# Performance work log

Measured on AMD Instinct MI355X. Metric: run time of the kernel, lower is better.

## Reference

```python
import jax, jax.numpy as jnp
import numpy as np

# Config mirroring RegionExtractor(__init__ defaults, stage='rcnn')
MIN_SIZE = 25.0
IOU_THRESH = 0.3
SCORE_THRESH = 0.001  # applied as box_score_thresh inside the wrapped FRCNN
MAX_DET = 100         # max_detections_per_image
IMG_SIZE = 800.0
B, N = 8, 2048


def setup_inputs() -> dict:
    key = jax.random.key(0)
    k_c, k_wh, k_s = jax.random.split(key, 3)
    # synthesize realistic xyxy boxes inside an 800x800 image
    centers = jax.random.uniform(k_c, (B, N, 2), minval=0.0, maxval=IMG_SIZE)
    wh = jax.random.uniform(k_wh, (B, N, 2), minval=1.0, maxval=250.0)
    x1y1 = jnp.clip(centers - wh / 2, 0.0, IMG_SIZE)
    x2y2 = jnp.clip(centers + wh / 2, 0.0, IMG_SIZE)
    boxes = jnp.concatenate([x1y1, x2y2], axis=-1).astype(jnp.float32)  # [B,N,4]
    scores = jax.random.uniform(k_s, (B, N), dtype=jnp.float32)          # [B,N]
    return {"boxes": boxes, "scores": scores}


def _box_iou(a, b):
    # a: [N,4], b: [N,4] xyxy -> [N,N] IoU (torchvision convention, no +1)
    area_a = (a[:, 2] - a[:, 0]) * (a[:, 3] - a[:, 1])
    area_b = (b[:, 2] - b[:, 0]) * (b[:, 3] - b[:, 1])
    lt = jnp.maximum(a[:, None, :2], b[None, :, :2])
    rb = jnp.minimum(a[:, None, 2:], b[None, :, 2:])
    wh = jnp.clip(rb - lt, 0.0)
    inter = wh[..., 0] * wh[..., 1]
    return inter / (area_a[:, None] + area_b[None, :] - inter)


def _process_image(boxes, scores):
    # boxes [N,4], scores [N] -> (out [K,4], mask [K])
    n = boxes.shape[0]
    w = boxes[:, 2] - boxes[:, 0]
    h = boxes[:, 3] - boxes[:, 1]
    # remove_small_boxes + score threshold (box_score_thresh in wrapped FRCNN)
    valid = (w >= MIN_SIZE) & (h >= MIN_SIZE) & (scores >= SCORE_THRESH)
    order = jnp.argsort(-jnp.where(valid, scores, -jnp.inf))  # desc, invalid last
    b = boxes[order]
    v = valid[order]
    sup = _box_iou(b, b) > IOU_THRESH  # [N,N]
    idx = jnp.arange(n)

    def body(i, keep):
        suppressed = jnp.any(keep & sup[:, i] & (idx < i))
        return keep.at[i].set(v[i] & ~suppressed)

    keep = jax.lax.fori_loop(0, n, body, jnp.zeros(n, dtype=bool))
    # keep is in score order already; take first MAX_DET kept boxes
    rank = jnp.cumsum(keep) - 1
    sel = keep & (rank < MAX_DET)
    tgt = jnp.where(sel, rank, MAX_DET)  # dump non-selected into scratch row
    out = jnp.zeros((MAX_DET + 1, 4), boxes.dtype).at[tgt].set(b)[:MAX_DET]
    num_kept = jnp.minimum(jnp.sum(keep), MAX_DET)
    mask = jnp.arange(MAX_DET) < num_kept
    return out, mask


def reference(boxes, scores):
    # Per-image filter + NMS + top-k, batched via vmap (padded fixed-shape output:
    # original returns a ragged [sum_k,5]; here rows with mask==False are padding).
    out, mask = jax.vmap(_process_image)(boxes, scores)  # [B,K,4], [B,K]
    b = boxes.shape[0]
    img_idx = jnp.repeat(jnp.arange(b, dtype=boxes.dtype), MAX_DET)[:, None]  # [B*K,1]
    regions = jnp.concatenate([img_idx, out.reshape(b * MAX_DET, 4)], axis=1)  # [B*K,5]
    return regions, mask.reshape(-1)
```

## Files before the change

### kernel.cpp

```cpp
#include <hip/hip_runtime.h>

#define NBOX   2048
#define HALF   1024
#define MAXDET 100
#define NIMG   8
#define POOL   256
#define IOU_MID 0x1.333335p-2

typedef unsigned long long u64;

__device__ __forceinline__ u64 shx64(u64 v, int m) {
    int lo = __shfl_xor((int)(unsigned int)v, m, 64);
    int hi = __shfl_xor((int)(unsigned int)(v >> 32), m, 64);
    return ((u64)(unsigned int)hi << 32) | (unsigned int)lo;
}
__device__ __forceinline__ u64 cmpsel(u64 mine, u64 part, bool take_max) {
    return ((mine > part) == take_max) ? mine : part;
}
__device__ __forceinline__ u64 readlane64(u64 v, int l) {
    unsigned int lo = (unsigned int)__builtin_amdgcn_readlane((int)(unsigned int)v, l);
    unsigned int hi = (unsigned int)__builtin_amdgcn_readlane((int)(v >> 32), l);
    return ((u64)hi << 32) | lo;
}
__device__ __forceinline__ u64 mkkey(float4 v, float s, int i) {
    bool valid = ((v.z - v.x) >= 25.0f) && ((v.w - v.y) >= 25.0f) && (s >= 0.001f);
    unsigned int sk = valid ? __float_as_uint(s) : 0u;
    return ((u64)sk << 32) | (unsigned int)(~i);
}

__global__ __launch_bounds__(1024) void k_all(
    const float* __restrict__ boxes, const float* __restrict__ scores,
    float* __restrict__ out)
{
    __shared__ u64    bufA[NBOX];
    __shared__ u64    bufB[NBOX];
    __shared__ u64    supRow[POOL * 4];
    __shared__ float4 sbox[POOL];
    __shared__ u64    mA[POOL], mB[POOL];
    __shared__ u64    validW[4];
    __shared__ u64    pminS;
    __shared__ int    kposL[MAXDET];
    __shared__ float4 leadersB[MAXDET];
    __shared__ float  leadersA[MAXDET];

    const int g    = threadIdx.x;
    const int lane = g & 63;
    const int wv   = g >> 6;
    const int tl   = g & 511;
    const int hbase = (g >> 9) * HALF;
    const int img  = blockIdx.x;
    const float4* bb4 = (const float4*)boxes + img * NBOX;
    const float*  ss  = scores + img * NBOX;

    const int e0 = 2 * tl;
    u64 k0, k1;
    { float4 v = bb4[hbase + e0];     k0 = mkkey(v, ss[hbase + e0],     hbase + e0);     }
    { float4 v = bb4[hbase + e0 + 1]; k1 = mkkey(v, ss[hbase + e0 + 1], hbase + e0 + 1); }

#define SWAP1(a, b, D) { if ((D) ? ((a) < (b)) : ((a) > (b))) { u64 t_ = (a); (a) = (b); (b) = t_; } }
    { bool D = ((tl & 1) == 0); SWAP1(k0, k1, D) }
    for (int KB = 2; KB <= 64; KB <<= 1) {
        bool D = ((tl & KB) == 0);
        for (int m = KB >> 1; m >= 1; m >>= 1) {
            bool tm = (D == ((lane & m) == 0));
            k0 = cmpsel(k0, shx64(k0, m), tm);
            k1 = cmpsel(k1, shx64(k1, m), tm);
        }
        SWAP1(k0, k1, D)
    }
    int sp = 0;
    for (int K = 256; K <= 1024; K <<= 1) {
        bool D = ((e0 & K) == 0);
        for (int j = K >> 1; j >= 128; j >>= 1) {
            u64* buf = (sp & 1) ? bufB : bufA;
            ++sp;
            buf[hbase + e0] = k0; buf[hbase + e0 + 1] = k1;
            __syncthreads();
            int pe = e0 ^ j;
            u64 p0 = buf[hbase + pe], p1 = buf[hbase + pe + 1];
            bool tm = (D == ((e0 & j) == 0));
            k0 = cmpsel(k0, p0, tm); k1 = cmpsel(k1, p1, tm);
        }
        for (int m = 32; m >= 1; m >>= 1) {
            bool tm = (D == ((lane & m) == 0));
            k0 = cmpsel(k0, shx64(k0, m), tm);
            k1 = cmpsel(k1, shx64(k1, m), tm);
        }
        SWAP1(k0, k1, D)
    }
    bufA[hbase + e0] = k0; bufA[hbase + e0 + 1] = k1;
    __syncthreads();

    const u64* hk = bufA;

    u64 c = 0;
    if (g < POOL) {
        u64 a  = hk[g];
        u64 bq = hk[HALF + (POOL - 1 - g)];
        c = (a > bq) ? a : bq;
        mA[g] = c;
    }
    __syncthreads();
    if (g < POOL) { c = cmpsel(c, mA[g ^ 128], (g & 128) == 0); mB[g] = c; }
    __syncthreads();
    if (g < POOL) {
        c = cmpsel(c, mB[g ^ 64], (g & 64) == 0);
        for (int m = 32; m >= 1; m >>= 1)
            c = cmpsel(c, shx64(c, m), (lane & m) == 0);
        unsigned int idx = ~(unsigned int)c;
        float4 v = bb4[idx];
        sbox[g] = v;
        u64 bal = __ballot(((unsigned int)(c >> 32)) != 0u);
        if (lane == 0) validW[wv] = bal;
        if (g == POOL - 1) pminS = c;
    }
    __syncthreads();

    float4 cb[4];
    float  ca[4];
#pragma unroll
    for (int w = 0; w < 4; ++w) {
        float4 v = sbox[(w << 6) + lane];
        cb[w] = v;
        ca[w] = (v.z - v.x) * (v.w - v.y);
    }

    for (int r = 0; r < POOL / 16; ++r) {
        int i = (r << 4) + wv;
        float4 Li = sbox[i];
        float La = (Li.z - Li.x) * (Li.w - Li.y);
        int w0 = i >> 6;
#pragma unroll
        for (int w = 0; w < 4; ++w) {
            if (w >= w0) {
                int j0 = (w << 6) + lane;
                float iw = fminf(Li.z, cb[w].z) - fmaxf(Li.x, cb[w].x);
                float ih = fminf(Li.w, cb[w].w) - fmaxf(Li.y, cb[w].y);
                iw = fmaxf(iw, 0.0f);
                ih = fmaxf(ih, 0.0f);
                float inter = iw * ih;
                float denom = (La + ca[w]) - inter;
                bool hit = (j0 > i) && ((double)inter > IOU_MID * (double)denom);
                u64 bits = __ballot(hit);
                if (lane == 0) supRow[(i << 2) + w] = bits;
            }
        }
    }
    __syncthreads();

    if (g >= 64) return;

    float* regions = out;
    float* maskv   = out + (size_t)NIMG * MAXDET * 5;

    u64 rd0 = supRow[(((0 << 6) + lane) << 2) + 0];
    u64 rd1 = supRow[(((1 << 6) + lane) << 2) + 1];
    u64 rd2 = supRow[(((2 << 6) + lane) << 2) + 2];
    u64 rd3 = supRow[(((3 << 6) + lane) << 2) + 3];

    int nkept = 0;
    u64 pend = 0;
#pragma unroll
    for (int s = 0; s < 4; ++s) {
        u64 rds = (s == 0) ? rd0 : (s == 1) ? rd1 : (s == 2) ? rd2 : rd3;
        u64 mcur = validW[s] & ~readlane64(pend, s);
        int n0 = nkept;
        while (mcur != 0ULL) {
            int il = (int)__builtin_ctzll(mcur);
            if (lane == 0) kposL[nkept] = (s << 6) + il;
            nkept++;
            if (nkept >= MAXDET) break;
            u64 rowS = readlane64(rds, il);
            mcur = (mcur & (mcur - 1)) & ~rowS;
        }
        if (nkept >= MAXDET) break;
        if (s < 3) {
            for (int t = n0 + (lane >> 2); t < nkept; t += 16)
                pend |= supRow[(kposL[t] << 2) + (lane & 3)];
            pend |= shx64(pend, 4);
            pend |= shx64(pend, 8);
            pend |= shx64(pend, 16);
            pend |= shx64(pend, 32);
        }
    }

    for (int t = lane; t < nkept; t += 64) {
        int ip = kposL[t];
        float4 v = sbox[ip];
        float* rr = regions + ((size_t)(img * MAXDET + t)) * 5;
        rr[0] = (float)img; rr[1] = v.x; rr[2] = v.y; rr[3] = v.z; rr[4] = v.w;
        maskv[img * MAXDET + t] = 1.0f;
        leadersB[t] = v;
        leadersA[t] = (v.z - v.x) * (v.w - v.y);
    }

    if (nkept < MAXDET) {
        u64 pmin = pminS;
        int q0 = 0, q1 = 0;
#pragma unroll
        for (int w = 0; w < 16; ++w) {
            q0 += __popcll(__ballot(hk[(w << 6) + lane] >= pmin));
            q1 += __popcll(__ballot(hk[HALF + (w << 6) + lane] >= pmin));
        }
        for (;;) {
            const int lenA = HALF - q0, lenB = HALF - q1;
            const int rem  = lenA + lenB;
            if (rem <= 0) break;
            u64  myKey = 0;
            bool fromA = false;
            if (lane < rem) {
                int lo = lane + 1 - lenB; if (lo < 0) lo = 0;
                int hi = (lane + 1 < lenA) ? lane + 1 : lenA;
                while (lo < hi) {
                    int a = (lo + hi) >> 1, b = lane + 1 - a;
                    if (a < lenA && b > 0 && hk[q0 + a] > hk[HALF + q1 + b - 1]) lo = a + 1;
                    else hi = a;
                }
                int a = lo, b = lane + 1 - a;
                u64 ka = (a > 0) ? hk[q0 + a - 1] : ~0ULL;
                u64 kb = (b > 0) ? hk[HALF + q1 + b - 1] : ~0ULL;
                fromA = (ka < kb);
                myKey = fromA ? ka : kb;
            }
            bool validC = (lane < rem) && (((unsigned int)(myKey >> 32)) != 0u);
            u64 vmask = __ballot(validC);
            float4 v = make_float4(0.0f, 0.0f, 0.0f, 0.0f);
            float varea = 0.0f;
            if (validC) {
                v = bb4[~(unsigned int)myKey];
                varea = (v.z - v.x) * (v.w - v.y);
            }
            bool supL = false;
#pragma unroll 4
            for (int t = 0; t < nkept; ++t) {
                float4 Lb = leadersB[t];
                float  La = leadersA[t];
                float iw = fminf(Lb.z, v.z) - fmaxf(Lb.x, v.x);
                float ih = fminf(Lb.w, v.w) - fmaxf(Lb.y, v.y);
                iw = fmaxf(iw, 0.0f);
                ih = fmaxf(ih, 0.0f);
                float inter = iw * ih;
                float denom = (La + varea) - inter;
                supL = supL || ((double)inter > IOU_MID * (double)denom);
            }
            u64 mcur = vmask & ~__ballot(supL);
            while (mcur != 0ULL) {
                int il = (int)__builtin_ctzll(mcur);
                float bx = __shfl(v.x, il, 64), by = __shfl(v.y, il, 64);
                float bz = __shfl(v.z, il, 64), bw = __shfl(v.w, il, 64);
                float ba = __shfl(varea, il, 64);
                if (lane == il) {
                    float* rr = regions + ((size_t)(img * MAXDET + nkept)) * 5;
                    rr[0] = (float)img; rr[1] = v.x; rr[2] = v.y; rr[3] = v.z; rr[4] = v.w;
                    maskv[img * MAXDET + nkept] = 1.0f;
                    leadersB[nkept] = v;
                    leadersA[nkept] = varea;
                }
                nkept++;
                if (nkept >= MAXDET) break;
                float iw = fminf(bz, v.z) - fmaxf(bx, v.x);
                float ih = fminf(bw, v.w) - fmaxf(by, v.y);
                iw = fmaxf(iw, 0.0f);
                ih = fmaxf(ih, 0.0f);
                float inter = iw * ih;
                float denom = (ba + varea) - inter;
                bool hit = ((double)inter > IOU_MID * (double)denom);
                mcur = (mcur & (mcur - 1)) & ~__ballot(hit);
            }
            if (nkept >= MAXDET) break;
            int nv = __popcll(vmask);
            if (nv < 64) break;
            int nA = __popcll(vmask & __ballot(fromA));
            q0 += nA;
            q1 += nv - nA;
        }
    }

    for (int r = nkept + lane; r < MAXDET; r += 64) {
        float* rr = regions + ((size_t)(img * MAXDET + r)) * 5;
        rr[0] = (float)img; rr[1] = 0.0f; rr[2] = 0.0f; rr[3] = 0.0f; rr[4] = 0.0f;
        maskv[img * MAXDET + r] = 0.0f;
    }
}

extern "C" void kernel_launch(void* const* d_in, const int* in_sizes, int n_in,
                              void* d_out, int out_size, void* d_ws, size_t ws_size,
                              hipStream_t stream) {
    const float* boxes  = (const float*)d_in[0];
    const float* scores = (const float*)d_in[1];
    float* out = (float*)d_out;
    k_all<<<NIMG, 1024, 0, stream>>>(boxes, scores, out);
}
```

Before: 76.38 us.

## Sort four keys per thread with fewer barriers and stage boxes in LDS

The per-half bitonic sort now uses 512 threads holding four keys each. More compare steps happen in registers and wave shuffles, so fewer LDS exchange rounds and __syncthreads are needed. The other 512 threads copy all 2048 boxes of the image into shared memory at the same time, and the later gathers by sorted index read from LDS instead of global memory. This adds 32KB of LDS, which may limit occupancy, though there is only one block per image anyway. It also leaves half the block idle during the sort phase.

```diff
diff --git a/kernel.cpp b/kernel.cpp
--- a/kernel.cpp
+++ b/kernel.cpp
@@ -34,6 +34,7 @@
 {
     __shared__ u64    bufA[NBOX];
     __shared__ u64    bufB[NBOX];
+    __shared__ float4 boxLds[NBOX];
     __shared__ u64    supRow[POOL * 4];
     __shared__ float4 sbox[POOL];
     __shared__ u64    mA[POOL], mB[POOL];
@@ -46,49 +47,87 @@
     const int g    = threadIdx.x;
     const int lane = g & 63;
     const int wv   = g >> 6;
-    const int tl   = g & 511;
-    const int hbase = (g >> 9) * HALF;
     const int img  = blockIdx.x;
     const float4* bb4 = (const float4*)boxes + img * NBOX;
     const float*  ss  = scores + img * NBOX;
 
-    const int e0 = 2 * tl;
-    u64 k0, k1;
-    { float4 v = bb4[hbase + e0];     k0 = mkkey(v, ss[hbase + e0],     hbase + e0);     }
-    { float4 v = bb4[hbase + e0 + 1]; k1 = mkkey(v, ss[hbase + e0 + 1], hbase + e0 + 1); }
-
 #define SWAP1(a, b, D) { if ((D) ? ((a) < (b)) : ((a) > (b))) { u64 t_ = (a); (a) = (b); (b) = t_; } }
-    { bool D = ((tl & 1) == 0); SWAP1(k0, k1, D) }
-    for (int KB = 2; KB <= 64; KB <<= 1) {
-        bool D = ((tl & KB) == 0);
-        for (int m = KB >> 1; m >= 1; m >>= 1) {
-            bool tm = (D == ((lane & m) == 0));
-            k0 = cmpsel(k0, shx64(k0, m), tm);
-            k1 = cmpsel(k1, shx64(k1, m), tm);
-        }
-        SWAP1(k0, k1, D)
-    }
-    int sp = 0;
-    for (int K = 256; K <= 1024; K <<= 1) {
-        bool D = ((e0 & K) == 0);
-        for (int j = K >> 1; j >= 128; j >>= 1) {
-            u64* buf = (sp & 1) ? bufB : bufA;
-            ++sp;
-            buf[hbase + e0] = k0; buf[hbase + e0 + 1] = k1;
-            __syncthreads();
-            int pe = e0 ^ j;
-            u64 p0 = buf[hbase + pe], p1 = buf[hbase + pe + 1];
-            bool tm = (D == ((e0 & j) == 0));
-            k0 = cmpsel(k0, p0, tm); k1 = cmpsel(k1, p1, tm);
-        }
+
+    u64 k0 = 0, k1 = 0, k2 = 0, k3 = 0;
+    int u = 0, hb = 0, base = 0;
+    if (g < 512) {
+        u = g & 255; hb = (g >> 8) * HALF; base = hb + (u << 2);
+        float4 sc = *((const float4*)(ss + base));
+        { float4 v = bb4[base + 0]; k0 = mkkey(v, sc.x, base + 0); }
+        { float4 v = bb4[base + 1]; k1 = mkkey(v, sc.y, base + 1); }
+        { float4 v = bb4[base + 2]; k2 = mkkey(v, sc.z, base + 2); }
+        { float4 v = bb4[base + 3]; k3 = mkkey(v, sc.w, base + 3); }
+        SWAP1(k0, k1, true) SWAP1(k2, k3, false)
+        { bool D = ((u & 1) == 0); SWAP1(k0, k2, D) SWAP1(k1, k3, D) SWAP1(k0, k1, D) SWAP1(k2, k3, D) }
+        for (int K4 = 2; K4 <= 64; K4 <<= 1) {
+            bool D = ((u & K4) == 0);
+            for (int m = K4 >> 1; m >= 1; m >>= 1) {
+                bool tm = (D == ((lane & m) == 0));
+                k0 = cmpsel(k0, shx64(k0, m), tm); k1 = cmpsel(k1, shx64(k1, m), tm);
+                k2 = cmpsel(k2, shx64(k2, m), tm); k3 = cmpsel(k3, shx64(k3, m), tm);
+            }
+            SWAP1(k0, k2, D) SWAP1(k1, k3, D) SWAP1(k0, k1, D) SWAP1(k2, k3, D)
+        }
+        bufB[hb + u]       = k0;
+        bufB[hb + 256 + u] = k1;
+        bufB[hb + 512 + u] = k2;
+        bufB[hb + 768 + u] = k3;
+    } else {
+        int b0 = g - 512;
+        boxLds[b0]        = bb4[b0];
+        boxLds[b0 + 512]  = bb4[b0 + 512];
+        boxLds[b0 + 1024] = bb4[b0 + 1024];
+        boxLds[b0 + 1536] = bb4[b0 + 1536];
+    }
+    __syncthreads();
+    if (g < 512) {
+        bool D = ((u & 128) == 0);
+        int pu = u ^ 64;
+        bool tm = (D == ((u & 64) == 0));
+        k0 = cmpsel(k0, bufB[hb + pu], tm);       k1 = cmpsel(k1, bufB[hb + 256 + pu], tm);
+        k2 = cmpsel(k2, bufB[hb + 512 + pu], tm); k3 = cmpsel(k3, bufB[hb + 768 + pu], tm);
         for (int m = 32; m >= 1; m >>= 1) {
-            bool tm = (D == ((lane & m) == 0));
-            k0 = cmpsel(k0, shx64(k0, m), tm);
-            k1 = cmpsel(k1, shx64(k1, m), tm);
-        }
-        SWAP1(k0, k1, D)
-    }
-    bufA[hbase + e0] = k0; bufA[hbase + e0 + 1] = k1;
+            bool t2 = (D == ((lane & m) == 0));
+            k0 = cmpsel(k0, shx64(k0, m), t2); k1 = cmpsel(k1, shx64(k1, m), t2);
+            k2 = cmpsel(k2, shx64(k2, m), t2); k3 = cmpsel(k3, shx64(k3, m), t2);
+        }
+        SWAP1(k0, k2, D) SWAP1(k1, k3, D) SWAP1(k0, k1, D) SWAP1(k2, k3, D)
+        bufA[hb + u]       = k0;
+        bufA[hb + 256 + u] = k1;
+        bufA[hb + 512 + u] = k2;
+        bufA[hb + 768 + u] = k3;
+    }
+    __syncthreads();
+    if (g < 512) {
+        int pu = u ^ 128;
+        bool tm = ((u & 128) == 0);
+        k0 = cmpsel(k0, bufA[hb + pu], tm);       k1 = cmpsel(k1, bufA[hb + 256 + pu], tm);
+        k2 = cmpsel(k2, bufA[hb + 512 + pu], tm); k3 = cmpsel(k3, bufA[hb + 768 + pu], tm);
+        bufB[hb + u]       = k0;
+        bufB[hb + 256 + u] = k1;
+        bufB[hb + 512 + u] = k2;
+        bufB[hb + 768 + u] = k3;
+    }
+    __syncthreads();
+    if (g < 512) {
+        int pu = u ^ 64;
+        bool tm = ((u & 64) == 0);
+        k0 = cmpsel(k0, bufB[hb + pu], tm);       k1 = cmpsel(k1, bufB[hb + 256 + pu], tm);
+        k2 = cmpsel(k2, bufB[hb + 512 + pu], tm); k3 = cmpsel(k3, bufB[hb + 768 + pu], tm);
+        for (int m = 32; m >= 1; m >>= 1) {
+            bool t2 = ((lane & m) == 0);
+            k0 = cmpsel(k0, shx64(k0, m), t2); k1 = cmpsel(k1, shx64(k1, m), t2);
+            k2 = cmpsel(k2, shx64(k2, m), t2); k3 = cmpsel(k3, shx64(k3, m), t2);
+        }
+        SWAP1(k0, k2, true) SWAP1(k1, k3, true) SWAP1(k0, k1, true) SWAP1(k2, k3, true)
+        bufA[base + 0] = k0; bufA[base + 1] = k1;
+        bufA[base + 2] = k2; bufA[base + 3] = k3;
+    }
     __syncthreads();
 
     const u64* hk = bufA;
@@ -108,7 +147,7 @@
         for (int m = 32; m >= 1; m >>= 1)
             c = cmpsel(c, shx64(c, m), (lane & m) == 0);
         unsigned int idx = ~(unsigned int)c;
-        float4 v = bb4[idx];
+        float4 v = boxLds[idx];
         sbox[g] = v;
         u64 bal = __ballot(((unsigned int)(c >> 32)) != 0u);
         if (lane == 0) validW[wv] = bal;
@@ -227,7 +266,7 @@
             float4 v = make_float4(0.0f, 0.0f, 0.0f, 0.0f);
             float varea = 0.0f;
             if (validC) {
-                v = bb4[~(unsigned int)myKey];
+                v = boxLds[~(unsigned int)myKey];
                 varea = (v.z - v.x) * (v.w - v.y);
             }
             bool supL = false;
```

Result: no change. 77.04 us (+0.9%).

## Prefetch second 256-candidate pool in parallel and stage boxes in LDS

Applied to the files above, without the earlier changes.

Caches all input boxes in shared memory so later candidate lookups read LDS instead of global memory. Precomputes a second sorted pool of 256 candidates with the whole block, right after the first pool, so the single-wave tail phase can process up to four 64-wide batches without the serial merge-path search. The old merge loop stays as a fallback when the second pool is used up. The cost is extra LDS (about 36 KB more, which could hurt occupancy) and block-wide work on the second pool even when it is never needed.

```diff
diff --git a/kernel.cpp b/kernel.cpp
--- a/kernel.cpp
+++ b/kernel.cpp
@@ -34,11 +34,15 @@
 {
     __shared__ u64    bufA[NBOX];
     __shared__ u64    bufB[NBOX];
+    __shared__ float4 boxLds[NBOX];
     __shared__ u64    supRow[POOL * 4];
     __shared__ float4 sbox[POOL];
+    __shared__ float4 sbox2[POOL];
     __shared__ u64    mA[POOL], mB[POOL];
     __shared__ u64    validW[4];
-    __shared__ u64    pminS;
+    __shared__ u64    validW2[4];
+    __shared__ int    q0W[4];
+    __shared__ u64    pmin2S;
     __shared__ int    kposL[MAXDET];
     __shared__ float4 leadersB[MAXDET];
     __shared__ float  leadersA[MAXDET];
@@ -54,8 +58,8 @@
 
     const int e0 = 2 * tl;
     u64 k0, k1;
-    { float4 v = bb4[hbase + e0];     k0 = mkkey(v, ss[hbase + e0],     hbase + e0);     }
-    { float4 v = bb4[hbase + e0 + 1]; k1 = mkkey(v, ss[hbase + e0 + 1], hbase + e0 + 1); }
+    { float4 v = bb4[hbase + e0];     boxLds[hbase + e0]     = v; k0 = mkkey(v, ss[hbase + e0],     hbase + e0);     }
+    { float4 v = bb4[hbase + e0 + 1]; boxLds[hbase + e0 + 1] = v; k1 = mkkey(v, ss[hbase + e0 + 1], hbase + e0 + 1); }
 
 #define SWAP1(a, b, D) { if ((D) ? ((a) < (b)) : ((a) > (b))) { u64 t_ = (a); (a) = (b); (b) = t_; } }
     { bool D = ((tl & 1) == 0); SWAP1(k0, k1, D) }
@@ -108,13 +112,38 @@
         for (int m = 32; m >= 1; m >>= 1)
             c = cmpsel(c, shx64(c, m), (lane & m) == 0);
         unsigned int idx = ~(unsigned int)c;
-        float4 v = bb4[idx];
+        float4 v = boxLds[idx];
         sbox[g] = v;
         u64 bal = __ballot(((unsigned int)(c >> 32)) != 0u);
         if (lane == 0) validW[wv] = bal;
-        if (g == POOL - 1) pminS = c;
-    }
-    __syncthreads();
+        u64 balA = __ballot(idx < (unsigned int)HALF);
+        if (lane == 0) q0W[wv] = __popcll(balA);
+    }
+    __syncthreads();
+
+    u64 c2 = 0;
+    int q0g = 0;
+    if (g < POOL) {
+        q0g = q0W[0] + q0W[1] + q0W[2] + q0W[3];
+        int q1g = POOL - q0g;
+        u64 a  = hk[q0g + g];
+        u64 bq = hk[HALF + q1g + (POOL - 1 - g)];
+        c2 = (a > bq) ? a : bq;
+        mA[g] = c2;
+    }
+    __syncthreads();
+    if (g < POOL) { c2 = cmpsel(c2, mA[g ^ 128], (g & 128) == 0); mB[g] = c2; }
+    __syncthreads();
+    if (g < POOL) {
+        c2 = cmpsel(c2, mB[g ^ 64], (g & 64) == 0);
+        for (int m = 32; m >= 1; m >>= 1)
+            c2 = cmpsel(c2, shx64(c2, m), (lane & m) == 0);
+        unsigned int idx2 = ~(unsigned int)c2;
+        sbox2[g] = boxLds[idx2];
+        u64 bal2 = __ballot(((unsigned int)(c2 >> 32)) != 0u);
+        if (lane == 0) validW2[wv] = bal2;
+        if (g == POOL - 1) pmin2S = c2;
+    }
 
     float4 cb[4];
     float  ca[4];
@@ -195,41 +224,12 @@
     }
 
     if (nkept < MAXDET) {
-        u64 pmin = pminS;
-        int q0 = 0, q1 = 0;
-#pragma unroll
-        for (int w = 0; w < 16; ++w) {
-            q0 += __popcll(__ballot(hk[(w << 6) + lane] >= pmin));
-            q1 += __popcll(__ballot(hk[HALF + (w << 6) + lane] >= pmin));
-        }
-        for (;;) {
-            const int lenA = HALF - q0, lenB = HALF - q1;
-            const int rem  = lenA + lenB;
-            if (rem <= 0) break;
-            u64  myKey = 0;
-            bool fromA = false;
-            if (lane < rem) {
-                int lo = lane + 1 - lenB; if (lo < 0) lo = 0;
-                int hi = (lane + 1 < lenA) ? lane + 1 : lenA;
-                while (lo < hi) {
-                    int a = (lo + hi) >> 1, b = lane + 1 - a;
-                    if (a < lenA && b > 0 && hk[q0 + a] > hk[HALF + q1 + b - 1]) lo = a + 1;
-                    else hi = a;
-                }
-                int a = lo, b = lane + 1 - a;
-                u64 ka = (a > 0) ? hk[q0 + a - 1] : ~0ULL;
-                u64 kb = (b > 0) ? hk[HALF + q1 + b - 1] : ~0ULL;
-                fromA = (ka < kb);
-                myKey = fromA ? ka : kb;
-            }
-            bool validC = (lane < rem) && (((unsigned int)(myKey >> 32)) != 0u);
-            u64 vmask = __ballot(validC);
-            float4 v = make_float4(0.0f, 0.0f, 0.0f, 0.0f);
-            float varea = 0.0f;
-            if (validC) {
-                v = bb4[~(unsigned int)myKey];
-                varea = (v.z - v.x) * (v.w - v.y);
-            }
+        bool exhausted = false;
+        for (int b = 0; b < 4; ++b) {
+            u64 vm = validW2[b];
+            if (vm == 0ULL) { exhausted = true; break; }
+            float4 v = sbox2[(b << 6) + lane];
+            float varea = (v.z - v.x) * (v.w - v.y);
             bool supL = false;
 #pragma unroll 4
             for (int t = 0; t < nkept; ++t) {
@@ -243,7 +243,7 @@
                 float denom = (La + varea) - inter;
                 supL = supL || ((double)inter > IOU_MID * (double)denom);
             }
-            u64 mcur = vmask & ~__ballot(supL);
+            u64 mcur = vm & ~__ballot(supL);
             while (mcur != 0ULL) {
                 int il = (int)__builtin_ctzll(mcur);
                 float bx = __shfl(v.x, il, 64), by = __shfl(v.y, il, 64);
@@ -268,11 +268,89 @@
                 mcur = (mcur & (mcur - 1)) & ~__ballot(hit);
             }
             if (nkept >= MAXDET) break;
-            int nv = __popcll(vmask);
-            if (nv < 64) break;
-            int nA = __popcll(vmask & __ballot(fromA));
-            q0 += nA;
-            q1 += nv - nA;
+            if (__popcll(vm) < 64) { exhausted = true; break; }
+        }
+
+        if (nkept < MAXDET && !exhausted) {
+            u64 pmin = pmin2S;
+            int q0 = 0, q1 = 0;
+#pragma unroll
+            for (int w = 0; w < 16; ++w) {
+                q0 += __popcll(__ballot(hk[(w << 6) + lane] >= pmin));
+                q1 += __popcll(__ballot(hk[HALF + (w << 6) + lane] >= pmin));
+            }
+            for (;;) {
+                const int lenA = HALF - q0, lenB = HALF - q1;
+                const int rem  = lenA + lenB;
+                if (rem <= 0) break;
+                u64  myKey = 0;
+                bool fromA = false;
+                if (lane < rem) {
+                    int lo = lane + 1 - lenB; if (lo < 0) lo = 0;
+                    int hi = (lane + 1 < lenA) ? lane + 1 : lenA;
+                    while (lo < hi) {
+                        int a = (lo + hi) >> 1, b = lane + 1 - a;
+                        if (a < lenA && b > 0 && hk[q0 + a] > hk[HALF + q1 + b - 1]) lo = a + 1;
+                        else hi = a;
+                    }
+                    int a = lo, b = lane + 1 - a;
+                    u64 ka = (a > 0) ? hk[q0 + a - 1] : ~0ULL;
+                    u64 kb = (b > 0) ? hk[HALF + q1 + b - 1] : ~0ULL;
+                    fromA = (ka < kb);
+                    myKey = fromA ? ka : kb;
+                }
+                bool validC = (lane < rem) && (((unsigned int)(myKey >> 32)) != 0u);
+                u64 vmask = __ballot(validC);
+                float4 v = make_float4(0.0f, 0.0f, 0.0f, 0.0f);
+                float varea = 0.0f;
+                if (validC) {
+                    v = boxLds[~(unsigned int)myKey];
+                    varea = (v.z - v.x) * (v.w - v.y);
+                }
+                bool supL = false;
+#pragma unroll 4
+                for (int t = 0; t < nkept; ++t) {
+                    float4 Lb = leadersB[t];
+                    float  La = leadersA[t];
+                    float iw = fminf(Lb.z, v.z) - fmaxf(Lb.x, v.x);
+                    float ih = fminf(Lb.w, v.w) - fmaxf(Lb.y, v.y);
+                    iw = fmaxf(iw, 0.0f);
+                    ih = fmaxf(ih, 0.0f);
+                    float inter = iw * ih;
+                    float denom = (La + varea) - inter;
+                    supL = supL || ((double)inter > IOU_MID * (double)denom);
+                }
+                u64 mcur = vmask & ~__ballot(supL);
+                while (mcur != 0ULL) {
+                    int il = (int)__builtin_ctzll(mcur);
+                    float bx = __shfl(v.x, il, 64), by = __shfl(v.y, il, 64);
+                    float bz = __shfl(v.z, il, 64), bw = __shfl(v.w, il, 64);
+                    float ba = __shfl(varea, il, 64);
+                    if (lane == il) {
+                        float* rr = regions + ((size_t)(img * MAXDET + nkept)) * 5;
+                        rr[0] = (float)img; rr[1] = v.x; rr[2] = v.y; rr[3] = v.z; rr[4] = v.w;
+                        maskv[img * MAXDET + nkept] = 1.0f;
+                        leadersB[nkept] = v;
+                        leadersA[nkept] = varea;
+                    }
+                    nkept++;
+                    if (nkept >= MAXDET) break;
+                    float iw = fminf(bz, v.z) - fmaxf(bx, v.x);
+                    float ih = fminf(bw, v.w) - fmaxf(by, v.y);
+                    iw = fmaxf(iw, 0.0f);
+                    ih = fmaxf(ih, 0.0f);
+                    float inter = iw * ih;
+                    float denom = (ba + varea) - inter;
+                    bool hit = ((double)inter > IOU_MID * (double)denom);
+                    mcur = (mcur & (mcur - 1)) & ~__ballot(hit);
+                }
+                if (nkept >= MAXDET) break;
+                int nv = __popcll(vmask);
+                if (nv < 64) break;
+                int nA = __popcll(vmask & __ballot(fromA));
+                q0 += nA;
+                q1 += nv - nA;
+            }
         }
     }
 
```

After: 77.84 us. About the same (+1.9%).
